# Kernel tuning notes

Measured on AMD Instinct MI355X. Metric: run time of the kernel, lower is better.

Reference implementation:

```python
import jax, jax.numpy as jnp
import numpy as np
from jax import lax

EPS = 1e-5  # torch BatchNorm2d default eps


def _dwconv3x3(x, w):
    # x: [B,C,H,W], w: [C,1,3,3] depthwise kernel (feature_group_count=C)
    return lax.conv_general_dilated(
        x, w, window_strides=(1, 1), padding=((1, 1), (1, 1)),
        dimension_numbers=("NCHW", "OIHW", "NCHW"),
        feature_group_count=x.shape[1])


def setup_inputs() -> dict:
    key = jax.random.key(0)
    k1, k2, k3, k4 = jax.random.split(key, 4)
    B, C, H, W = 16, 256, 128, 128
    x = jax.random.normal(k1, (B, C, H, W), jnp.float32)
    dw_weight = jax.random.normal(k2, (C, 1, 3, 3), jnp.float32) * 0.1
    bn_gamma = jax.random.uniform(k3, (C,), jnp.float32, 0.5, 1.5)
    bn_beta = jax.random.normal(k4, (C,), jnp.float32) * 0.1
    bn_mean = jnp.zeros((C,), jnp.float32)
    bn_var = jnp.ones((C,), jnp.float32)
    return {"x": x, "dw_weight": dw_weight, "bn_gamma": bn_gamma,
            "bn_beta": bn_beta, "bn_mean": bn_mean, "bn_var": bn_var}


def reference(x, dw_weight, bn_gamma, bn_beta, bn_mean, bn_var):
    C = x.shape[1]
    sobel_x = jnp.array([[-1, 0, 1], [-2, 0, 2], [-1, 0, 1]], jnp.float32)
    sobel_y = jnp.array([[-1, -2, -1], [0, 0, 0], [1, 2, 1]], jnp.float32)
    kx = jnp.tile(sobel_x[None, None], (C, 1, 1, 1))  # [C,1,3,3]
    ky = jnp.tile(sobel_y[None, None], (C, 1, 1, 1))
    # per-channel Sobel (original Python loop == depthwise conv with shared kernel)
    gx = _dwconv3x3(x, kx)
    gy = _dwconv3x3(x, ky)
    edge = (jnp.abs(gx) + jnp.abs(gy)) * 0.5
    # depthwise conv + BN (eval mode) + ReLU
    y = _dwconv3x3(edge, dw_weight)
    inv = bn_gamma / jnp.sqrt(bn_var + EPS)
    y = y * inv[None, :, None, None] + (bn_beta - bn_mean * inv)[None, :, None, None]
    return jax.nn.relu(y)
```

## Files before the change

kernel.cpp:

```cpp
#include <hip/hip_runtime.h>
#include <cstddef>


#define BB 16
#define CC 256
#define HH 128
#define WW 128
#define TY 16
#define XROWS (TY + 4)
#define EROWS (TY + 2)
#define XSTR 136
#define EPS 1e-5f

__global__ __launch_bounds__(256) void edge_attn_fused(
    const float* __restrict__ x,
    const float* __restrict__ dw,
    const float* __restrict__ gamma,
    const float* __restrict__ beta,
    const float* __restrict__ mean,
    const float* __restrict__ var,
    float* __restrict__ out)
{
    __shared__ __align__(16) float sx[XROWS * XSTR];
    __shared__ __align__(16) float se[EROWS * XSTR];

    const int tid  = threadIdx.x;
    const int tile = blockIdx.x & 7;
    const int bc   = blockIdx.x >> 3;
    const int c    = bc & (CC - 1);
    const int y0   = tile * TY;

    const float* __restrict__ xp = x + (size_t)bc * (HH * WW);

    for (int i = tid; i < XROWS * 32; i += 256) {
        int r  = i >> 5;
        int c4 = i & 31;
        int gr = y0 - 2 + r;
        float4 v = make_float4(0.f, 0.f, 0.f, 0.f);
        if ((unsigned)gr < (unsigned)HH)
            v = *(const float4*)(xp + gr * WW + (c4 << 2));
        *(float4*)(&sx[r * XSTR + 4 + (c4 << 2)]) = v;
    }
    if (tid < XROWS * 4) {
        int r = tid >> 2, k = tid & 3;
        sx[r * XSTR + ((k < 2) ? (2 + k) : (130 + k))] = 0.f;
    }
    if (tid >= 128 && tid < 128 + EROWS * 2) {
        int t = tid - 128;
        se[(t >> 1) * XSTR + ((t & 1) ? 132 : 3)] = 0.f;
    }
    __syncthreads();

    for (int i = tid; i < EROWS * 32; i += 256) {
        int r   = i >> 5;
        int c4  = i & 31;
        int ger = y0 - 1 + r;
        float4 ev = make_float4(0.f, 0.f, 0.f, 0.f);
        if ((unsigned)ger < (unsigned)HH) {
            const float* p0 = &sx[r * XSTR + 4 + (c4 << 2)];
            const float* p1 = p0 + XSTR;
            const float* p2 = p0 + 2 * XSTR;
            float4 m0 = *(const float4*)p0; float lt0 = p0[-1], rt0 = p0[4];
            float4 m1 = *(const float4*)p1; float lt1 = p1[-1], rt1 = p1[4];
            float4 m2 = *(const float4*)p2; float lt2 = p2[-1], rt2 = p2[4];
            #define SOB(a0l,a0c,a0r,a1l,a1r,a2l,a2c,a2r) \
                (0.5f * (fabsf(((a0r)-(a0l)) + 2.f*((a1r)-(a1l)) + ((a2r)-(a2l))) \
                       + fabsf(((a2l)-(a0l)) + 2.f*((a2c)-(a0c)) + ((a2r)-(a0r)))))
            ev.x = SOB(lt0, m0.x, m0.y,  lt1, m1.y,  lt2, m2.x, m2.y);
            ev.y = SOB(m0.x, m0.y, m0.z, m1.x, m1.z, m2.x, m2.y, m2.z);
            ev.z = SOB(m0.y, m0.z, m0.w, m1.y, m1.w, m2.y, m2.z, m2.w);
            ev.w = SOB(m0.z, m0.w, rt0,  m1.z, rt1,  m2.z, m2.w, rt2);
            #undef SOB
        }
        *(float4*)(&se[r * XSTR + 4 + (c4 << 2)]) = ev;
    }
    __syncthreads();

    const float* __restrict__ wp = dw + c * 9;
    const float w0 = wp[0], w1 = wp[1], w2 = wp[2];
    const float w3 = wp[3], w4 = wp[4], w5 = wp[5];
    const float w6 = wp[6], w7 = wp[7], w8 = wp[8];
    const float inv  = gamma[c] / sqrtf(var[c] + EPS);
    const float bias = beta[c] - mean[c] * inv;

    float* __restrict__ op = out + (size_t)bc * (HH * WW) + y0 * WW;

    for (int i = tid; i < TY * 32; i += 256) {
        int r  = i >> 5;
        int c4 = i & 31;
        const float* p0 = &se[r * XSTR + 4 + (c4 << 2)];
        const float* p1 = p0 + XSTR;
        const float* p2 = p0 + 2 * XSTR;
        float4 m0 = *(const float4*)p0; float lt0 = p0[-1], rt0 = p0[4];
        float4 m1 = *(const float4*)p1; float lt1 = p1[-1], rt1 = p1[4];
        float4 m2 = *(const float4*)p2; float lt2 = p2[-1], rt2 = p2[4];
        float4 o;
        o.x = w0*lt0  + w1*m0.x + w2*m0.y + w3*lt1  + w4*m1.x + w5*m1.y + w6*lt2  + w7*m2.x + w8*m2.y;
        o.y = w0*m0.x + w1*m0.y + w2*m0.z + w3*m1.x + w4*m1.y + w5*m1.z + w6*m2.x + w7*m2.y + w8*m2.z;
        o.z = w0*m0.y + w1*m0.z + w2*m0.w + w3*m1.y + w4*m1.z + w5*m1.w + w6*m2.y + w7*m2.z + w8*m2.w;
        o.w = w0*m0.z + w1*m0.w + w2*rt0  + w3*m1.z + w4*m1.w + w5*rt1  + w6*m2.z + w7*m2.w + w8*rt2;
        o.x = fmaxf(o.x * inv + bias, 0.f);
        o.y = fmaxf(o.y * inv + bias, 0.f);
        o.z = fmaxf(o.z * inv + bias, 0.f);
        o.w = fmaxf(o.w * inv + bias, 0.f);
        *(float4*)(op + r * WW + (c4 << 2)) = o;
    }
}

extern "C" void kernel_launch(void* const* d_in, const int* in_sizes, int n_in,
                              void* d_out, int out_size, void* d_ws, size_t ws_size,
                              hipStream_t stream) {
    const float* x     = (const float*)d_in[0];
    const float* dw    = (const float*)d_in[1];
    const float* gamma = (const float*)d_in[2];
    const float* beta  = (const float*)d_in[3];
    const float* mean  = (const float*)d_in[4];
    const float* var   = (const float*)d_in[5];
    float* out = (float*)d_out;

    const int nblocks = BB * CC * (HH / TY);
    edge_attn_fused<<<nblocks, 256, 0, stream>>>(x, dw, gamma, beta, mean, var, out);
}
```

Measured before the change: 472.6 us.

## Replace shared-memory tiles with register-resident rolling row window per wavefront

Each 64-lane wavefront now owns a 64-row strip of one channel plane and streams down it, keeping a rolling window of x rows, separable Sobel partials and edge rows in registers. Horizontal neighbours come from cross-lane shuffles instead of LDS, which removes the shared-memory staging, both block barriers and the recomputed halo rows of the 16-row tiles. In exchange, each wave has a serial loop of 64 dependent row iterations with only one row prefetched ahead, so less memory parallelism is exposed per wave. Loads shrink to float2 per lane.

```diff
diff --git a/kernel.cpp b/kernel.cpp
--- a/kernel.cpp
+++ b/kernel.cpp
@@ -6,13 +6,53 @@
 #define CC 256
 #define HH 128
 #define WW 128
-#define TY 16
-#define XROWS (TY + 4)
-#define EROWS (TY + 2)
-#define XSTR 136
+#define RSTRIP 64
+#define NSTRIP (HH / RSTRIP)
 #define EPS 1e-5f
 
-__global__ __launch_bounds__(256) void edge_attn_fused(
+struct DS { float dA, dB, sA, sB; };
+struct ER { float el, eA, eB, er; };
+
+__device__ __forceinline__ void xrow_load(const float* __restrict__ xp, int j,
+                                          int lane, float& a0, float& a1) {
+    if ((unsigned)j < (unsigned)HH) {
+        const float2 v = *(const float2*)(xp + (size_t)j * WW + (lane << 1));
+        a0 = v.x; a1 = v.y;
+    } else {
+        a0 = 0.f; a1 = 0.f;
+    }
+}
+
+__device__ __forceinline__ DS make_ds(float a0, float a1, int lane) {
+    float xl = __shfl(a1, lane - 1, 64);
+    float xr = __shfl(a0, lane + 1, 64);
+    xl = (lane == 0)  ? 0.f : xl;
+    xr = (lane == 63) ? 0.f : xr;
+    DS d;
+    d.dA = a1 - xl;
+    d.dB = xr - a0;
+    d.sA = xl + 2.f * a0 + a1;
+    d.sB = a0 + 2.f * a1 + xr;
+    return d;
+}
+
+__device__ __forceinline__ ER make_edge(const DS& p, const DS& q, const DS& t,
+                                        int lane) {
+    float gxA = p.dA + 2.f * q.dA + t.dA;
+    float gxB = p.dB + 2.f * q.dB + t.dB;
+    float gyA = t.sA - p.sA;
+    float gyB = t.sB - p.sB;
+    ER e;
+    e.eA = 0.5f * (fabsf(gxA) + fabsf(gyA));
+    e.eB = 0.5f * (fabsf(gxB) + fabsf(gyB));
+    float el = __shfl(e.eB, lane - 1, 64);
+    float er = __shfl(e.eA, lane + 1, 64);
+    e.el = (lane == 0)  ? 0.f : el;
+    e.er = (lane == 63) ? 0.f : er;
+    return e;
+}
+
+__global__ __launch_bounds__(256) void edge_attn_reg(
     const float* __restrict__ x,
     const float* __restrict__ dw,
     const float* __restrict__ gamma,
@@ -21,60 +61,14 @@
     const float* __restrict__ var,
     float* __restrict__ out)
 {
-    __shared__ __align__(16) float sx[XROWS * XSTR];
-    __shared__ __align__(16) float se[EROWS * XSTR];
+    const int lane = threadIdx.x & 63;
+    const int wid  = (blockIdx.x << 2) + (threadIdx.x >> 6);
+    const int bc   = wid >> 1;
+    const int y0   = (wid & 1) * RSTRIP;
+    const int c    = bc & (CC - 1);
 
-    const int tid  = threadIdx.x;
-    const int tile = blockIdx.x & 7;
-    const int bc   = blockIdx.x >> 3;
-    const int c    = bc & (CC - 1);
-    const int y0   = tile * TY;
-
-    const float* __restrict__ xp = x + (size_t)bc * (HH * WW);
-
-    for (int i = tid; i < XROWS * 32; i += 256) {
-        int r  = i >> 5;
-        int c4 = i & 31;
-        int gr = y0 - 2 + r;
-        float4 v = make_float4(0.f, 0.f, 0.f, 0.f);
-        if ((unsigned)gr < (unsigned)HH)
-            v = *(const float4*)(xp + gr * WW + (c4 << 2));
-        *(float4*)(&sx[r * XSTR + 4 + (c4 << 2)]) = v;
-    }
-    if (tid < XROWS * 4) {
-        int r = tid >> 2, k = tid & 3;
-        sx[r * XSTR + ((k < 2) ? (2 + k) : (130 + k))] = 0.f;
-    }
-    if (tid >= 128 && tid < 128 + EROWS * 2) {
-        int t = tid - 128;
-        se[(t >> 1) * XSTR + ((t & 1) ? 132 : 3)] = 0.f;
-    }
-    __syncthreads();
-
-    for (int i = tid; i < EROWS * 32; i += 256) {
-        int r   = i >> 5;
-        int c4  = i & 31;
-        int ger = y0 - 1 + r;
-        float4 ev = make_float4(0.f, 0.f, 0.f, 0.f);
-        if ((unsigned)ger < (unsigned)HH) {
-            const float* p0 = &sx[r * XSTR + 4 + (c4 << 2)];
-            const float* p1 = p0 + XSTR;
-            const float* p2 = p0 + 2 * XSTR;
-            float4 m0 = *(const float4*)p0; float lt0 = p0[-1], rt0 = p0[4];
-            float4 m1 = *(const float4*)p1; float lt1 = p1[-1], rt1 = p1[4];
-            float4 m2 = *(const float4*)p2; float lt2 = p2[-1], rt2 = p2[4];
-            #define SOB(a0l,a0c,a0r,a1l,a1r,a2l,a2c,a2r) \
-                (0.5f * (fabsf(((a0r)-(a0l)) + 2.f*((a1r)-(a1l)) + ((a2r)-(a2l))) \
-                       + fabsf(((a2l)-(a0l)) + 2.f*((a2c)-(a0c)) + ((a2r)-(a0r)))))
-            ev.x = SOB(lt0, m0.x, m0.y,  lt1, m1.y,  lt2, m2.x, m2.y);
-            ev.y = SOB(m0.x, m0.y, m0.z, m1.x, m1.z, m2.x, m2.y, m2.z);
-            ev.z = SOB(m0.y, m0.z, m0.w, m1.y, m1.w, m2.y, m2.z, m2.w);
-            ev.w = SOB(m0.z, m0.w, rt0,  m1.z, rt1,  m2.z, m2.w, rt2);
-            #undef SOB
-        }
-        *(float4*)(&se[r * XSTR + 4 + (c4 << 2)]) = ev;
-    }
-    __syncthreads();
+    const float* __restrict__ xp = x   + (size_t)bc * (HH * WW);
+    float* __restrict__       op = out + (size_t)bc * (HH * WW);
 
     const float* __restrict__ wp = dw + c * 9;
     const float w0 = wp[0], w1 = wp[1], w2 = wp[2];
@@ -83,27 +77,50 @@
     const float inv  = gamma[c] / sqrtf(var[c] + EPS);
     const float bias = beta[c] - mean[c] * inv;
 
-    float* __restrict__ op = out + (size_t)bc * (HH * WW) + y0 * WW;
+    float ta0, ta1, tb0, tb1, tc0, tc1, td0, td1, xa, xb;
+    xrow_load(xp, y0 - 2, lane, ta0, ta1);
+    xrow_load(xp, y0 - 1, lane, tb0, tb1);
+    xrow_load(xp, y0,     lane, tc0, tc1);
+    xrow_load(xp, y0 + 1, lane, td0, td1);
+    xrow_load(xp, y0 + 2, lane, xa, xb);
 
-    for (int i = tid; i < TY * 32; i += 256) {
-        int r  = i >> 5;
-        int c4 = i & 31;
-        const float* p0 = &se[r * XSTR + 4 + (c4 << 2)];
-        const float* p1 = p0 + XSTR;
-        const float* p2 = p0 + 2 * XSTR;
-        float4 m0 = *(const float4*)p0; float lt0 = p0[-1], rt0 = p0[4];
-        float4 m1 = *(const float4*)p1; float lt1 = p1[-1], rt1 = p1[4];
-        float4 m2 = *(const float4*)p2; float lt2 = p2[-1], rt2 = p2[4];
-        float4 o;
-        o.x = w0*lt0  + w1*m0.x + w2*m0.y + w3*lt1  + w4*m1.x + w5*m1.y + w6*lt2  + w7*m2.x + w8*m2.y;
-        o.y = w0*m0.x + w1*m0.y + w2*m0.z + w3*m1.x + w4*m1.y + w5*m1.z + w6*m2.x + w7*m2.y + w8*m2.z;
-        o.z = w0*m0.y + w1*m0.z + w2*m0.w + w3*m1.y + w4*m1.z + w5*m1.w + w6*m2.y + w7*m2.z + w8*m2.w;
-        o.w = w0*m0.z + w1*m0.w + w2*rt0  + w3*m1.z + w4*m1.w + w5*rt1  + w6*m2.z + w7*m2.w + w8*rt2;
-        o.x = fmaxf(o.x * inv + bias, 0.f);
-        o.y = fmaxf(o.y * inv + bias, 0.f);
-        o.z = fmaxf(o.z * inv + bias, 0.f);
-        o.w = fmaxf(o.w * inv + bias, 0.f);
-        *(float4*)(op + r * WW + (c4 << 2)) = o;
+    DS dsA = make_ds(ta0, ta1, lane);
+    DS dsB = make_ds(tb0, tb1, lane);
+    DS d0  = make_ds(tc0, tc1, lane);
+    DS d1  = make_ds(td0, td1, lane);
+
+    ER e_m;
+    if (y0 > 0) e_m = make_edge(dsA, dsB, d0, lane);
+    else        { e_m.el = e_m.eA = e_m.eB = e_m.er = 0.f; }
+    ER e_c = make_edge(dsB, d0, d1, lane);
+
+    const int jlim = (y0 + RSTRIP + 1 < HH) ? (y0 + RSTRIP + 1) : (HH - 1);
+
+    for (int r = y0; r < y0 + RSTRIP; ++r) {
+        float na, nb;
+        int j = r + 3;
+        if (j <= jlim) xrow_load(xp, j, lane, na, nb);
+        else           { na = 0.f; nb = 0.f; }
+
+        DS d2 = make_ds(xa, xb, lane);
+
+        ER e_p;
+        if (r + 1 < HH) e_p = make_edge(d0, d1, d2, lane);
+        else            { e_p.el = e_p.eA = e_p.eB = e_p.er = 0.f; }
+
+        float o0 = w0 * e_m.el + w1 * e_m.eA + w2 * e_m.eB
+                 + w3 * e_c.el + w4 * e_c.eA + w5 * e_c.eB
+                 + w6 * e_p.el + w7 * e_p.eA + w8 * e_p.eB;
+        float o1 = w0 * e_m.eA + w1 * e_m.eB + w2 * e_m.er
+                 + w3 * e_c.eA + w4 * e_c.eB + w5 * e_c.er
+                 + w6 * e_p.eA + w7 * e_p.eB + w8 * e_p.er;
+        o0 = fmaxf(o0 * inv + bias, 0.f);
+        o1 = fmaxf(o1 * inv + bias, 0.f);
+        *(float2*)(op + (size_t)r * WW + (lane << 1)) = make_float2(o0, o1);
+
+        d0 = d1; d1 = d2;
+        e_m = e_c; e_c = e_p;
+        xa = na; xb = nb;
     }
 }
 
@@ -118,6 +135,6 @@
     const float* var   = (const float*)d_in[5];
     float* out = (float*)d_out;
 
-    const int nblocks = BB * CC * (HH / TY);
-    edge_attn_fused<<<nblocks, 256, 0, stream>>>(x, dw, gamma, beta, mean, var, out);
+    const int nblocks = (BB * CC * NSTRIP) / 4;
+    edge_attn_reg<<<nblocks, 256, 0, stream>>>(x, dw, gamma, beta, mean, var, out);
 }
```

After: 448.7 us. 5.1% less time.
